# Optimization experiments

Measured on AMD Instinct MI355X. Metric: run time of the kernel, lower is better.

Reference implementation:

```python
import jax, jax.numpy as jnp
import numpy as np

H = 32        # query heads
KV = 8        # kv heads (GQA)
D = 128       # head_dim
HID = 4096    # hidden_size
T = 2048      # tokens (single causal sequence)
THETA = 10000.0


def setup_inputs() -> dict:
    key = jax.random.key(0)
    k1, k2, k3 = jax.random.split(key, 3)
    return {
        "positions": jnp.arange(T, dtype=jnp.int32),
        "hidden_states": jax.random.normal(k1, (T, HID), dtype=jnp.float32),
        "w_qkv": jax.random.normal(k2, ((H + 2 * KV) * D, HID), dtype=jnp.float32) * 0.02,
        "w_o": jax.random.normal(k3, (HID, H * D), dtype=jnp.float32) * 0.02,
    }


def _rope_neox(x, cos, sin):
    # x: [T, h, D]; cos/sin: [T, D/2]
    half = x.shape[-1] // 2
    x1, x2 = x[..., :half], x[..., half:]
    c, s = cos[:, None, :], sin[:, None, :]
    return jnp.concatenate([x1 * c - x2 * s, x2 * c + x1 * s], axis=-1)


def reference(positions, hidden_states, w_qkv, w_o):
    t = hidden_states.shape[0]
    qkv = hidden_states @ w_qkv.T                      # [T, (H+2KV)*D]
    q, k, v = jnp.split(qkv, [H * D, H * D + KV * D], axis=-1)
    q = q.reshape(t, H, D)
    k = k.reshape(t, KV, D)
    v = v.reshape(t, KV, D)

    # neox-style RoPE over full head_dim
    half = D // 2
    inv_freq = 1.0 / (THETA ** (jnp.arange(0, D, 2, dtype=jnp.float32) / D))  # [D/2]
    freqs = positions.astype(jnp.float32)[:, None] * inv_freq                 # [T, D/2]
    cos, sin = jnp.cos(freqs), jnp.sin(freqs)
    q = _rope_neox(q, cos, sin)
    k = _rope_neox(k, cos, sin)

    # GQA: expand kv heads to match query heads
    rep = H // KV
    k = jnp.repeat(k, rep, axis=1)                     # [T, H, D]
    v = jnp.repeat(v, rep, axis=1)

    scale = D ** -0.5
    scores = jnp.einsum('thd,shd->hts', q, k) * scale  # [H, T, T]
    causal = positions[:, None] >= positions[None, :]  # [T, T]
    neg = jnp.finfo(scores.dtype).min
    scores = jnp.where(causal[None], scores, neg)
    attn = jax.nn.softmax(scores, axis=-1)
    out = jnp.einsum('hts,shd->thd', attn, v).reshape(t, H * D)
    return out @ w_o.T                                 # [T, HID]
```

## Files before the change

kernel.cpp:

```cpp
#include <hip/hip_runtime.h>
#include <hip/hip_bf16.h>
#include <cstdint>

typedef __bf16 bf16;
typedef __bf16 bf16x8 __attribute__((ext_vector_type(8)));
typedef float f32x4 __attribute__((ext_vector_type(4)));

#define DEV __device__ __forceinline__

DEV f32x4 mfma16(bf16x8 a, bf16x8 b, f32x4 c) {
  return __builtin_amdgcn_mfma_f32_16x16x32_bf16(a, b, c, 0, 0, 0);
}

DEV void gl2lds16(const void* g, void* l) {
  __builtin_amdgcn_global_load_lds((__attribute__((address_space(1))) void*)g,
                                   (__attribute__((address_space(3))) void*)l,
                                   16, 0, 0);
}

DEV void cvt8(const float* __restrict__ s, bf16* __restrict__ d) {
  f32x4 a = *(const f32x4*)(s);
  f32x4 b = *(const f32x4*)(s + 4);
  bf16x8 o;
#pragma unroll
  for (int e = 0; e < 4; ++e) { o[e] = (bf16)a[e]; o[e + 4] = (bf16)b[e]; }
  *(bf16x8*)(d) = o;
}

__global__ void cvt3(const float* __restrict__ s0, bf16* __restrict__ d0, int n0,
                     const float* __restrict__ s1, bf16* __restrict__ d1, int n1,
                     const float* __restrict__ s2, bf16* __restrict__ d2) {
  long i = ((long)blockIdx.x * 256 + threadIdx.x) * 8;
  if (i < n0) { cvt8(s0 + i, d0 + i); return; }
  i -= n0;
  if (i < n1) { cvt8(s1 + i, d1 + i); return; }
  i -= n1;
  cvt8(s2 + i, d2 + i);
}

template <typename OutT, int SPLIT>
DEV void gemm_body(const bf16* __restrict__ A, const bf16* __restrict__ B,
                   OutT* __restrict__ C, int M, int N, int K) {
  __shared__ bf16 As[2 * 128 * 32];
  __shared__ bf16 Bs[2 * 128 * 32];
  const int tid = threadIdx.x;
  const int lane = tid & 63, w = tid >> 6;
  const int wm = w & 1, wn = w >> 1;
  const int quad = lane >> 4, r = lane & 15;
  const long mBase = (long)blockIdx.y * 128, nBase = (long)blockIdx.x * 128;
  const int Kh = K / SPLIT;
  const int kBeg = blockIdx.z * Kh, kEnd = kBeg + Kh;
  f32x4 acc[4][4];
#pragma unroll
  for (int i = 0; i < 4; ++i)
#pragma unroll
    for (int j = 0; j < 4; ++j) acc[i][j] = f32x4{0.f, 0.f, 0.f, 0.f};

  for (int k0 = kBeg; k0 < kEnd; k0 += 64) {
    __syncthreads();
#pragma unroll
    for (int j = 0; j < 4; ++j) {
      const int c = w * 256 + j * 64 + lane;
      const int half = c >> 9, row = (c >> 2) & 127, k4 = c & 3;
      const long koff = k0 + half * 32 + k4 * 8;
      gl2lds16(A + (mBase + row) * (long)K + koff, (char*)As + (w * 256 + j * 64) * 16);
      gl2lds16(B + (nBase + row) * (long)K + koff, (char*)Bs + (w * 256 + j * 64) * 16);
    }
    __syncthreads();
#pragma unroll
    for (int h = 0; h < 2; ++h) {
      bf16x8 af[4], bfr[4];
#pragma unroll
      for (int i = 0; i < 4; ++i) {
        af[i]  = *(const bf16x8*)(&As[h * 4096 + (wm * 64 + i * 16 + r) * 32 + quad * 8]);
        bfr[i] = *(const bf16x8*)(&Bs[h * 4096 + (wn * 64 + i * 16 + r) * 32 + quad * 8]);
      }
#pragma unroll
      for (int mi = 0; mi < 4; ++mi)
#pragma unroll
        for (int ni = 0; ni < 4; ++ni)
          acc[mi][ni] = mfma16(af[mi], bfr[ni], acc[mi][ni]);
    }
  }
  OutT* Cz = C + (size_t)blockIdx.z * M * N;
#pragma unroll
  for (int mi = 0; mi < 4; ++mi)
#pragma unroll
    for (int ni = 0; ni < 4; ++ni)
#pragma unroll
      for (int rg = 0; rg < 4; ++rg) {
        long row = mBase + wm * 64 + mi * 16 + quad * 4 + rg;
        long col = nBase + wn * 64 + ni * 16 + r;
        Cz[row * N + col] = (OutT)acc[mi][ni][rg];
      }
}

__global__ __launch_bounds__(256) void gemm_qkv(const bf16* __restrict__ A,
                                                const bf16* __restrict__ B,
                                                bf16* __restrict__ C, int M, int N, int K) {
  gemm_body<bf16, 1>(A, B, C, M, N, K);
}

__global__ __launch_bounds__(256) void gemm_out2(const bf16* __restrict__ A,
                                                 const bf16* __restrict__ B,
                                                 float* __restrict__ C, int M, int N, int K) {
  gemm_body<float, 2>(A, B, C, M, N, K);
}

__global__ void reduce_add(const float* __restrict__ p, float* __restrict__ o, int n) {
  const int i = (blockIdx.x * 256 + threadIdx.x) * 8;
  const f32x4 a0 = *(const f32x4*)(p + i),     b0 = *(const f32x4*)(p + n + i);
  const f32x4 a1 = *(const f32x4*)(p + i + 4), b1 = *(const f32x4*)(p + n + i + 4);
  *(f32x4*)(o + i) = a0 + b0;
  *(f32x4*)(o + i + 4) = a1 + b1;
}

__global__ void rope_kernel(bf16* __restrict__ qkv, const int* __restrict__ pos) {
  int idx = blockIdx.x * 256 + threadIdx.x;
  int g = idx & 7;
  int rest = idx >> 3;
  int head = rest % 40;
  int t = rest / 40;
  bf16* p = qkv + (long)t * 6144 + head * 128 + g * 8;
  bf16x8 a = *(const bf16x8*)(p);
  bf16x8 b = *(const bf16x8*)(p + 64);
  const float pf = (float)pos[t];
  bf16x8 oa, ob;
#pragma unroll
  for (int e = 0; e < 8; ++e) {
    const int d = g * 8 + e;
    const float invf = __builtin_expf(-(float)d * (9.210340371976184f / 64.0f));
    const float fr = pf * invf;
    const float c = __builtin_cosf(fr), s = __builtin_sinf(fr);
    const float x1 = (float)a[e], x2 = (float)b[e];
    oa[e] = (bf16)(x1 * c - x2 * s);
    ob[e] = (bf16)(x2 * c + x1 * s);
  }
  *(bf16x8*)(p) = oa;
  *(bf16x8*)(p + 64) = ob;
}

__global__ __launch_bounds__(256, 2) void attn_kernel(const bf16* __restrict__ qkv,
                                                      bf16* __restrict__ out) {
  constexpr int LDV = 72, LDP = 72;
  constexpr float SCL2 = 0.08838834764831845f * 1.4426950408889634f;
  __shared__ bf16 Ks[2][64 * 128];
  __shared__ bf16 Vt[2][128 * LDV];
  __shared__ bf16 Ps[64 * LDP];
  const int tid = threadIdx.x;
  const int lane = tid & 63, w = tid >> 6;
  const int quad = lane >> 4, r = lane & 15;
  const int pr = blockIdx.x, h = blockIdx.y;
  const int kvh = h >> 2;

  bf16x8 kreg[4], vreg[4];
  int srow[4], sdc[4];
#pragma unroll
  for (int ii = 0; ii < 4; ++ii) {
    const int c = ii * 256 + tid;
    srow[ii] = c >> 4;
    sdc[ii] = c & 15;
  }

  for (int which = 0; which < 2; ++which) {
    const int qt = which ? (31 - pr) : pr;
    const int rowq = qt * 64 + w * 16;

    bf16x8 qf[4];
#pragma unroll
    for (int ks = 0; ks < 4; ++ks)
      qf[ks] = *(const bf16x8*)(qkv + (long)(rowq + r) * 6144 + h * 128 + ks * 32 + quad * 8);

    f32x4 of[8];
#pragma unroll
    for (int di = 0; di < 8; ++di) of[di] = f32x4{0.f, 0.f, 0.f, 0.f};
    float mrun[4], lrun[4];
#pragma unroll
    for (int rg = 0; rg < 4; ++rg) { mrun[rg] = -__builtin_inff(); lrun[rg] = 0.f; }

    const int ntiles = qt + 1;
#pragma unroll
    for (int ii = 0; ii < 4; ++ii) {
      const long rb = (long)srow[ii] * 6144 + kvh * 128;
      kreg[ii] = *(const bf16x8*)(qkv + rb + 4096 + sdc[ii] * 8);
      vreg[ii] = *(const bf16x8*)(qkv + rb + 5120 + sdc[ii] * 8);
    }

    for (int kt = 0; kt < ntiles; ++kt) {
      const int kvbase = kt * 64;
      const int buf = kt & 1;
#pragma unroll
      for (int ii = 0; ii < 4; ++ii) {
        const int row = srow[ii], dc = sdc[ii];
        *(bf16x8*)(&Ks[buf][row * 128 + ((dc ^ (row & 15)) << 3)]) = kreg[ii];
        const int pc = (((row >> 3) ^ (dc & 7)) << 3) + (row & 7);
#pragma unroll
        for (int e = 0; e < 8; ++e) Vt[buf][(dc * 8 + e) * LDV + pc] = vreg[ii][e];
      }
      {
        const int kvn = (kt + 1 < ntiles) ? (kt + 1) * 64 : kt * 64;
#pragma unroll
        for (int ii = 0; ii < 4; ++ii) {
          const long rb = (long)(kvn + srow[ii]) * 6144 + kvh * 128;
          kreg[ii] = *(const bf16x8*)(qkv + rb + 4096 + sdc[ii] * 8);
          vreg[ii] = *(const bf16x8*)(qkv + rb + 5120 + sdc[ii] * 8);
        }
      }
      __syncthreads();

      f32x4 sacc[4];
#pragma unroll
      for (int ni = 0; ni < 4; ++ni) sacc[ni] = f32x4{0.f, 0.f, 0.f, 0.f};
#pragma unroll
      for (int ks = 0; ks < 4; ++ks) {
        bf16x8 kf[4];
#pragma unroll
        for (int ni = 0; ni < 4; ++ni)
          kf[ni] = *(const bf16x8*)(&Ks[buf][(ni * 16 + r) * 128 + (((ks * 4 + quad) ^ r) << 3)]);
#pragma unroll
        for (int ni = 0; ni < 4; ++ni) sacc[ni] = mfma16(qf[ks], kf[ni], sacc[ni]);
      }

      float mt[4];
#pragma unroll
      for (int rg = 0; rg < 4; ++rg) mt[rg] = -1e30f;
      if (kt == qt) {
        const int rq = rowq + quad * 4;
#pragma unroll
        for (int ni = 0; ni < 4; ++ni) {
          const int ck = kvbase + ni * 16 + r;
#pragma unroll
          for (int rg = 0; rg < 4; ++rg) {
            float sv = sacc[ni][rg];
            sv = (ck > rq + rg) ? -1e30f : sv;
            sacc[ni][rg] = sv;
            mt[rg] = fmaxf(mt[rg], sv);
          }
        }
      } else {
#pragma unroll
        for (int ni = 0; ni < 4; ++ni)
#pragma unroll
          for (int rg = 0; rg < 4; ++rg) mt[rg] = fmaxf(mt[rg], sacc[ni][rg]);
      }
#pragma unroll
      for (int rg = 0; rg < 4; ++rg) {
        float v = mt[rg];
        v = fmaxf(v, __shfl_xor(v, 1));
        v = fmaxf(v, __shfl_xor(v, 2));
        v = fmaxf(v, __shfl_xor(v, 4));
        v = fmaxf(v, __shfl_xor(v, 8));
        mt[rg] = v;
      }
      float alpha[4], rsum[4];
#pragma unroll
      for (int rg = 0; rg < 4; ++rg) {
        const float mnew = fmaxf(mrun[rg], mt[rg]);
        alpha[rg] = __builtin_exp2f((mrun[rg] - mnew) * SCL2);
        mrun[rg] = mnew;
        rsum[rg] = 0.f;
      }
#pragma unroll
      for (int ni = 0; ni < 4; ++ni)
#pragma unroll
        for (int rg = 0; rg < 4; ++rg) {
          const float pv = __builtin_exp2f((sacc[ni][rg] - mrun[rg]) * SCL2);
          rsum[rg] += pv;
          Ps[(w * 16 + quad * 4 + rg) * LDP + ni * 16 + r] = (bf16)pv;
        }
#pragma unroll
      for (int rg = 0; rg < 4; ++rg) {
        float v = rsum[rg];
        v += __shfl_xor(v, 1);
        v += __shfl_xor(v, 2);
        v += __shfl_xor(v, 4);
        v += __shfl_xor(v, 8);
        lrun[rg] = lrun[rg] * alpha[rg] + v;
      }
#pragma unroll
      for (int di = 0; di < 8; ++di)
#pragma unroll
        for (int rg = 0; rg < 4; ++rg) of[di][rg] *= alpha[rg];

#pragma unroll
      for (int js = 0; js < 2; ++js) {
        const bf16x8 pf = *(const bf16x8*)(&Ps[(w * 16 + r) * LDP + js * 32 + quad * 8]);
#pragma unroll
        for (int di = 0; di < 8; ++di) {
          const int vrow = di * 16 + r;
          const int vcol = (((js * 4 + quad) ^ ((vrow >> 3) & 7)) << 3);
          const bf16x8 vf = *(const bf16x8*)(&Vt[buf][vrow * LDV + vcol]);
          of[di] = mfma16(pf, vf, of[di]);
        }
      }
    }

#pragma unroll
    for (int rg = 0; rg < 4; ++rg) {
      const float inv = 1.f / lrun[rg];
      const long t = rowq + quad * 4 + rg;
#pragma unroll
      for (int di = 0; di < 8; ++di)
        out[t * 4096 + h * 128 + di * 16 + r] = (bf16)(of[di][rg] * inv);
    }
  }
}

extern "C" void kernel_launch(void* const* d_in, const int* in_sizes, int n_in,
                              void* d_out, int out_size, void* d_ws, size_t ws_size,
                              hipStream_t stream) {
  const int* positions = (const int*)d_in[0];
  const float* hidden = (const float*)d_in[1];
  const float* w_qkv = (const float*)d_in[2];
  const float* w_o = (const float*)d_in[3];
  float* out = (float*)d_out;

  char* ws = (char*)d_ws;
  bf16* hid_b  = (bf16*)(ws);
  bf16* wqkv_b = (bf16*)(ws + 16777216);
  bf16* wo_b   = (bf16*)(ws + 67108864);
  bf16* qkv    = (bf16*)(ws + 100663296);
  bf16* attn   = (bf16*)(ws + 125829120);
  float* part  = (float*)(ws);

  cvt3<<<24576, 256, 0, stream>>>(hidden, hid_b, 8388608,
                                  w_qkv, wqkv_b, 25165824,
                                  w_o, wo_b);
  gemm_qkv<<<dim3(48, 16), 256, 0, stream>>>(hid_b, wqkv_b, qkv, 2048, 6144, 4096);
  rope_kernel<<<2560, 256, 0, stream>>>(qkv, positions);
  attn_kernel<<<dim3(16, 32), 256, 0, stream>>>(qkv, attn);
  gemm_out2<<<dim3(32, 16, 2), 256, 0, stream>>>(attn, wo_b, part, 2048, 4096, 4096);
  reduce_add<<<4096, 256, 0, stream>>>(part, out, 8388608);
}
```

Baseline: 552.8 us.

## Rewrite projection GEMMs as 256x256 tiles with 4-stage LDS pipeline

```diff
diff --git a/kernel.cpp b/kernel.cpp
--- a/kernel.cpp
+++ b/kernel.cpp
@@ -17,6 +17,8 @@
                                    (__attribute__((address_space(3))) void*)l,
                                    16, 0, 0);
 }
+
+#define VMWAIT(N) asm volatile("s_waitcnt vmcnt(" #N ")" ::: "memory")
 
 DEV void cvt8(const float* __restrict__ s, bf16* __restrict__ d) {
   f32x4 a = *(const f32x4*)(s);
@@ -39,72 +41,97 @@
 }
 
 template <typename OutT, int SPLIT>
-DEV void gemm_body(const bf16* __restrict__ A, const bf16* __restrict__ B,
-                   OutT* __restrict__ C, int M, int N, int K) {
-  __shared__ bf16 As[2 * 128 * 32];
-  __shared__ bf16 Bs[2 * 128 * 32];
+DEV void gemm256_body(const bf16* __restrict__ A, const bf16* __restrict__ B,
+                      OutT* __restrict__ C, int M, int N, int K) {
+  __shared__ char lds[131072];
   const int tid = threadIdx.x;
   const int lane = tid & 63, w = tid >> 6;
-  const int wm = w & 1, wn = w >> 1;
+  const int wm = w >> 2, wn = w & 3;
   const int quad = lane >> 4, r = lane & 15;
-  const long mBase = (long)blockIdx.y * 128, nBase = (long)blockIdx.x * 128;
+  const long mBase = (long)blockIdx.y * 256, nBase = (long)blockIdx.x * 256;
   const int Kh = K / SPLIT;
-  const int kBeg = blockIdx.z * Kh, kEnd = kBeg + Kh;
-  f32x4 acc[4][4];
-#pragma unroll
-  for (int i = 0; i < 4; ++i)
+  const long kBeg = (long)blockIdx.z * Kh;
+  const int G = Kh >> 5;
+
+  const bf16* src[4];
+#pragma unroll
+  for (int i = 0; i < 4; ++i) {
+    const int c = i * 512 + tid;
+    const int part = c >> 10, row = (c >> 2) & 255, slot = c & 3;
+    const int kc = slot ^ ((row >> 1) & 3);
+    const bf16* base = part ? (B + (nBase + row) * (long)K)
+                            : (A + (mBase + row) * (long)K);
+    src[i] = base + kBeg + kc * 8;
+  }
+
+  const int pslot = (quad ^ ((r >> 1) & 3)) << 4;
+  const int offA = (wm * 128 + r) * 64 + pslot;
+  const int offB = 16384 + (wn * 64 + r) * 64 + pslot;
+
+  f32x4 acc[8][4];
+#pragma unroll
+  for (int i = 0; i < 8; ++i)
 #pragma unroll
     for (int j = 0; j < 4; ++j) acc[i][j] = f32x4{0.f, 0.f, 0.f, 0.f};
 
-  for (int k0 = kBeg; k0 < kEnd; k0 += 64) {
-    __syncthreads();
-#pragma unroll
-    for (int j = 0; j < 4; ++j) {
-      const int c = w * 256 + j * 64 + lane;
-      const int half = c >> 9, row = (c >> 2) & 127, k4 = c & 3;
-      const long koff = k0 + half * 32 + k4 * 8;
-      gl2lds16(A + (mBase + row) * (long)K + koff, (char*)As + (w * 256 + j * 64) * 16);
-      gl2lds16(B + (nBase + row) * (long)K + koff, (char*)Bs + (w * 256 + j * 64) * 16);
-    }
-    __syncthreads();
-#pragma unroll
-    for (int h = 0; h < 2; ++h) {
-      bf16x8 af[4], bfr[4];
-#pragma unroll
-      for (int i = 0; i < 4; ++i) {
-        af[i]  = *(const bf16x8*)(&As[h * 4096 + (wm * 64 + i * 16 + r) * 32 + quad * 8]);
-        bfr[i] = *(const bf16x8*)(&Bs[h * 4096 + (wn * 64 + i * 16 + r) * 32 + quad * 8]);
-      }
-#pragma unroll
-      for (int mi = 0; mi < 4; ++mi)
-#pragma unroll
-        for (int ni = 0; ni < 4; ++ni)
-          acc[mi][ni] = mfma16(af[mi], bfr[ni], acc[mi][ni]);
-    }
-  }
+  auto stage = [&](int p) {
+    char* db = lds + ((p & 3) << 15);
+    const long ko = (long)p * 32;
+#pragma unroll
+    for (int i = 0; i < 4; ++i)
+      gl2lds16(src[i] + ko, db + (i * 512 + w * 64) * 16);
+  };
+
+  auto phase = [&](int p, bool do_stage) {
+    __builtin_amdgcn_s_barrier();
+    __builtin_amdgcn_sched_barrier(0);
+    char* rb = lds + ((p & 3) << 15);
+    bf16x8 af[8], bfr[4];
+#pragma unroll
+    for (int mi = 0; mi < 8; ++mi) af[mi] = *(const bf16x8*)(rb + offA + mi * 1024);
+#pragma unroll
+    for (int ni = 0; ni < 4; ++ni) bfr[ni] = *(const bf16x8*)(rb + offB + ni * 1024);
+    if (do_stage) stage(p + 3);
+    asm volatile("s_waitcnt lgkmcnt(0)" ::: "memory");
+    __builtin_amdgcn_sched_barrier(0);
+    __builtin_amdgcn_s_setprio(1);
+#pragma unroll
+    for (int mi = 0; mi < 8; ++mi)
+#pragma unroll
+      for (int ni = 0; ni < 4; ++ni)
+        acc[mi][ni] = mfma16(af[mi], bfr[ni], acc[mi][ni]);
+    __builtin_amdgcn_s_setprio(0);
+  };
+
+  stage(0); stage(1); stage(2);
+  for (int p = 0; p < G - 3; ++p) { VMWAIT(8); phase(p, true); }
+  VMWAIT(8); phase(G - 3, false);
+  VMWAIT(4); phase(G - 2, false);
+  VMWAIT(0); phase(G - 1, false);
+
   OutT* Cz = C + (size_t)blockIdx.z * M * N;
 #pragma unroll
-  for (int mi = 0; mi < 4; ++mi)
+  for (int mi = 0; mi < 8; ++mi)
 #pragma unroll
     for (int ni = 0; ni < 4; ++ni)
 #pragma unroll
       for (int rg = 0; rg < 4; ++rg) {
-        long row = mBase + wm * 64 + mi * 16 + quad * 4 + rg;
+        long row = mBase + wm * 128 + mi * 16 + quad * 4 + rg;
         long col = nBase + wn * 64 + ni * 16 + r;
         Cz[row * N + col] = (OutT)acc[mi][ni][rg];
       }
 }
 
-__global__ __launch_bounds__(256) void gemm_qkv(const bf16* __restrict__ A,
-                                                const bf16* __restrict__ B,
-                                                bf16* __restrict__ C, int M, int N, int K) {
-  gemm_body<bf16, 1>(A, B, C, M, N, K);
-}
-
-__global__ __launch_bounds__(256) void gemm_out2(const bf16* __restrict__ A,
-                                                 const bf16* __restrict__ B,
-                                                 float* __restrict__ C, int M, int N, int K) {
-  gemm_body<float, 2>(A, B, C, M, N, K);
+__global__ __launch_bounds__(512, 2) void gemm_qkv(const bf16* __restrict__ A,
+                                                   const bf16* __restrict__ B,
+                                                   bf16* __restrict__ C, int M, int N, int K) {
+  gemm256_body<bf16, 1>(A, B, C, M, N, K);
+}
+
+__global__ __launch_bounds__(512, 2) void gemm_out2(const bf16* __restrict__ A,
+                                                    const bf16* __restrict__ B,
+                                                    float* __restrict__ C, int M, int N, int K) {
+  gemm256_body<float, 2>(A, B, C, M, N, K);
 }
 
 __global__ void reduce_add(const float* __restrict__ p, float* __restrict__ o, int n) {
@@ -326,9 +353,9 @@
   cvt3<<<24576, 256, 0, stream>>>(hidden, hid_b, 8388608,
                                   w_qkv, wqkv_b, 25165824,
                                   w_o, wo_b);
-  gemm_qkv<<<dim3(48, 16), 256, 0, stream>>>(hid_b, wqkv_b, qkv, 2048, 6144, 4096);
+  gemm_qkv<<<dim3(24, 8), 512, 0, stream>>>(hid_b, wqkv_b, qkv, 2048, 6144, 4096);
   rope_kernel<<<2560, 256, 0, stream>>>(qkv, positions);
   attn_kernel<<<dim3(16, 32), 256, 0, stream>>>(qkv, attn);
-  gemm_out2<<<dim3(32, 16, 2), 256, 0, stream>>>(attn, wo_b, part, 2048, 4096, 4096);
+  gemm_out2<<<dim3(16, 8, 2), 512, 0, stream>>>(attn, wo_b, part, 2048, 4096, 4096);
   reduce_add<<<4096, 256, 0, stream>>>(part, out, 8388608);
 }
```

Result: no change. 549.1 us (-0.7%).
